# Kernel tuning notes

Hardware: AMD Instinct MI355X
Metric: run time of the kernel (lower is better)

The kernel has to match this reference:

```python
import jax, jax.numpy as jnp
import numpy as np

# Directable[TL_table[i]] for i = 0..7: (dx, dy) with dx=horizontal shift, dy=vertical shift
# dx=+1 -> shift right (zero-fill col 0), dx=-1 -> shift left; dy=+1 -> shift down, dy=-1 -> shift up.
DIRS = [(1, 1), (0, 1), (-1, 1), (1, 0), (-1, 0), (1, -1), (0, -1), (-1, -1)]


def _shift(img, dx, dy):
    # img: [B, H, W]; zero-padded shift equivalent to bmm with the sparse translation matrices
    if dx == 1:
        img = jnp.pad(img[..., :-1], ((0, 0), (0, 0), (1, 0)))
    elif dx == -1:
        img = jnp.pad(img[..., 1:], ((0, 0), (0, 0), (0, 1)))
    if dy == 1:
        img = jnp.pad(img[:, :-1, :], ((0, 0), (1, 0), (0, 0)))
    elif dy == -1:
        img = jnp.pad(img[:, 1:, :], ((0, 0), (0, 1), (0, 0)))
    return img


def _bce(p, t):
    # torch F.binary_cross_entropy clamps log terms at -100
    logp = jnp.maximum(jnp.log(p), -100.0)
    log1mp = jnp.maximum(jnp.log(1.0 - p), -100.0)
    return -jnp.mean(t * logp + (1.0 - t) * log1mp)


def setup_inputs() -> dict:
    key = jax.random.key(0)
    k1, k2, k3 = jax.random.split(key, 3)
    B, C, H, W = 16, 8, 512, 512
    c_map = jax.random.normal(k1, (B, C, H, W), dtype=jnp.float32)
    target = jax.random.randint(k2, (B, 1, H, W), 0, 2, dtype=jnp.int32)
    con_target = jax.random.randint(k3, (B, C, H, W), 0, 2, dtype=jnp.int32)
    return {"c_map": c_map, "target": target, "con_target": con_target}


def reference(c_map, target, con_target):
    target = target.astype(jnp.float32)        # [B,1,H,W]
    con_target = con_target.astype(jnp.float32)  # [B,8,H,W]

    p = jax.nn.sigmoid(c_map)  # [B,8,H,W]

    # Bilateral voting: shifted[i] = shift(p[:, 7-i]) in direction DIRS[i]
    shifted = jnp.stack(
        [_shift(p[:, 7 - i], dx, dy) for i, (dx, dy) in enumerate(DIRS)], axis=1
    )  # [B,8,H,W]
    vote_out = p * shifted                       # [B,8,H,W] (== bimap.squeeze(1))
    final_pred = jnp.max(vote_out, axis=1, keepdims=True)  # [B,1,H,W]

    # dice loss (sums over dims (1,2) of the 4D tensors, as in the original)
    smooth = 0.001
    i_sum = jnp.sum(target, axis=(1, 2))
    j_sum = jnp.sum(final_pred, axis=(1, 2))
    inter = jnp.sum(target * final_pred, axis=(1, 2))
    loss_dice = jnp.mean(1.0 - (2.0 * inter + smooth) / (i_sum + j_sum + smooth))

    # edge (decouple) loss
    sum_conn = jnp.sum(con_target, axis=1)  # [B,H,W]
    edge = ((sum_conn < 8) & (sum_conn > 0)).astype(p.dtype)
    pred_min = jnp.min(vote_out, axis=1) * edge
    decouple_loss = _bce(pred_min, jnp.zeros_like(pred_min))

    bce_loss = _bce(final_pred, target)
    conmap_l = _bce(p, con_target)
    bimap_l = _bce(vote_out, con_target)

    return 0.8 * conmap_l + decouple_loss + 0.2 * bimap_l + bce_loss + loss_dice
```

## Files before the change

### kernel.cpp

```cpp
#include <hip/hip_runtime.h>

namespace {
constexpr int Bn = 16, Hn = 512, Wn = 512;
constexpr int HW  = Hn * Wn;
constexpr int CHW = 8 * HW;
constexpr int NCOL = Bn * Wn;
constexpr int ROWS = 8;
constexpr int GX   = Hn / ROWS;
constexpr int NBLK = GX * Bn;
constexpr int FBLK = 32;

__device__ __forceinline__ float frcp(float x) { return __builtin_amdgcn_rcpf(x); }

typedef float f4u __attribute__((ext_vector_type(4), aligned(4)));
}


__global__ __launch_bounds__(256, 4) void bicon_main(
    const float* __restrict__ c_map,
    const int*   __restrict__ target,
    const int*   __restrict__ con_target,
    float* __restrict__ col_i, float* __restrict__ col_j, float* __restrict__ col_x,
    double* __restrict__ bscal)
{
    const int tid  = threadIdx.x;
    const int lane = tid & 63;
    const int wv   = tid >> 6;
    const int half = wv & 1;
    const int rofs = wv >> 1;
    const int b    = blockIdx.y;
    const int h0   = blockIdx.x * ROWS;
    const int wq   = half * 256 + lane * 4;

    const float* cm = c_map      + (size_t)b * CHW;
    const int*   ct = con_target + (size_t)b * CHW;
    const int*   tg = target     + (size_t)b * HW;

    float s_con = 0.f, s_bi = 0.f, s_bce = 0.f, s_dec = 0.f;
    float ci[4] = {0, 0, 0, 0}, cj[4] = {0, 0, 0, 0}, cx[4] = {0, 0, 0, 0};

#pragma unroll 1
    for (int r = 0; r < ROWS / 2; ++r) {
        const int h    = h0 + 2 * r + rofs;
        const int base = h * Wn + wq;

        unsigned lo = 0u;
#pragma unroll
        for (int c = 0; c < 8; ++c) {
            const int4 u = *(const int4*)(ct + c * HW + base);
            lo |= ((unsigned)u.x << c)        | ((unsigned)u.y << (8 + c)) |
                  ((unsigned)u.z << (16 + c)) | ((unsigned)u.w << (24 + c));
        }

        float vmax[4], vmin[4];
#pragma unroll
        for (int k = 0; k < 4; ++k) { vmax[k] = 0.f; vmin[k] = 2.f; }

        auto center = [&](int c, float s[4]) {
            const float4 v = *(const float4*)(cm + c * HW + base);
            const float xs[4] = {v.x, v.y, v.z, v.w};
#pragma unroll
            for (int k = 0; k < 4; ++k) {
                const float e = __expf(-xs[k]);
                const float d = 1.f + e;
                s[k] = frcp(d);
                const float logd = __logf(d);
                s_con += fmaxf(((lo >> (8 * k + c)) & 1u) ? -logd : (-xs[k] - logd),
                               -100.f);
            }
        };
        auto nbr = [&](int c, int dy, int dx, float n[4]) {
            const int hn = h + dy;
            if ((unsigned)hn < (unsigned)Hn) {
                const f4u v = *(const f4u*)(cm + c * HW + hn * Wn + (wq + dx));
                const float xs[4] = {v.x, v.y, v.z, v.w};
#pragma unroll
                for (int k = 0; k < 4; ++k) n[k] = frcp(1.f + __expf(-xs[k]));
                if (dx == 1 && wq == Wn - 4) n[3] = 0.f;
                if (dx == -1 && wq == 0)     n[0] = 0.f;
            } else {
#pragma unroll
                for (int k = 0; k < 4; ++k) n[k] = 0.f;
            }
        };
        auto vote = [&](int i, const float si[4], const float nn[4]) {
#pragma unroll
            for (int k = 0; k < 4; ++k) {
                const float v = si[k] * nn[k];
                vmax[k] = fmaxf(vmax[k], v);
                vmin[k] = fminf(vmin[k], v);
                s_bi += fmaxf(__logf(((lo >> (8 * k + i)) & 1u) ? v : 1.f - v),
                              -100.f);
            }
        };

        {
            float pa[4], pb[4], na[4], nb_[4];
            center(0, pa); center(7, pb);
            nbr(0, +1, +1, na);  vote(7, pb, na);
            nbr(7, -1, -1, nb_); vote(0, pa, nb_);
        }
        {
            float pa[4], pb[4], na[4], nb_[4];
            center(1, pa); center(6, pb);
            nbr(1, +1, 0, na);   vote(6, pb, na);
            nbr(6, -1, 0, nb_);  vote(1, pa, nb_);
        }
        {
            float pa[4], pb[4], na[4], nb_[4];
            center(2, pa); center(5, pb);
            nbr(2, +1, -1, na);  vote(5, pb, na);
            nbr(5, -1, +1, nb_); vote(2, pa, nb_);
        }
        {
            float pa[4], pb[4], na[4], nb_[4];
            center(3, pa); center(4, pb);
            nbr(3, 0, +1, na);   vote(4, pb, na);
            nbr(4, 0, -1, nb_);  vote(3, pa, nb_);
        }

        const int4 t = *(const int4*)(tg + base);
        const int tk[4] = {t.x, t.y, t.z, t.w};
#pragma unroll
        for (int k = 0; k < 4; ++k) {
            const float fm = vmax[k];
            s_bce += fmaxf(__logf(tk[k] ? fm : 1.f - fm), -100.f);
            const int sc = __popc((int)((lo >> (8 * k)) & 0xffu));
            s_dec += (sc > 0 && sc < 8) ? fmaxf(__logf(1.f - vmin[k]), -100.f) : 0.f;
            ci[k] += (float)tk[k];
            cj[k] += fm;
            cx[k] += tk[k] ? fm : 0.f;
        }
    }

    __shared__ float cred[3][4][256];
#pragma unroll
    for (int k = 0; k < 4; ++k) {
        cred[0][wv][(lane << 2) + k] = ci[k];
        cred[1][wv][(lane << 2) + k] = cj[k];
        cred[2][wv][(lane << 2) + k] = cx[k];
    }

#pragma unroll
    for (int off = 32; off > 0; off >>= 1) {
        s_con += __shfl_down(s_con, off);
        s_bi  += __shfl_down(s_bi,  off);
        s_bce += __shfl_down(s_bce, off);
        s_dec += __shfl_down(s_dec, off);
    }
    __shared__ float wred[4][4];
    if (lane == 0) {
        wred[wv][0] = s_con; wred[wv][1] = s_bi;
        wred[wv][2] = s_bce; wred[wv][3] = s_dec;
    }
    __syncthreads();

#pragma unroll
    for (int j = tid; j < 512; j += 256) {
        const int hj = j >> 8, cidx = j & 255;
        const float a0 = cred[0][hj][cidx] + cred[0][hj + 2][cidx];
        const float a1 = cred[1][hj][cidx] + cred[1][hj + 2][cidx];
        const float a2 = cred[2][hj][cidx] + cred[2][hj + 2][cidx];
        atomicAdd(&col_i[b * Wn + j], a0);
        atomicAdd(&col_j[b * Wn + j], a1);
        atomicAdd(&col_x[b * Wn + j], a2);
    }
    if (tid < 4) {
        bscal[((size_t)blockIdx.y * GX + blockIdx.x) * 4 + tid] =
            (double)(wred[0][tid] + wred[1][tid] + wred[2][tid] + wred[3][tid]);
    }
}

__global__ __launch_bounds__(256) void bicon_finish(
    const float* __restrict__ col_i,
    const float* __restrict__ col_j,
    const float* __restrict__ col_x,
    const double* __restrict__ bscal,
    float* __restrict__ out)
{
    const int tid = threadIdx.x;
    const int col = blockIdx.x * 256 + tid;

    double part;
    {
        const float fi = col_i[col], fj = col_j[col], fx = col_x[col];
        part = (1.0 - (2.0 * (double)fx + 0.001) /
                      ((double)fi + (double)fj + 0.001)) / 8192.0;
    }
    if (tid < 32) {
        const int s = blockIdx.x * 32 + tid;
        const double c0 = bscal[s * 4 + 0], c1 = bscal[s * 4 + 1];
        const double c2 = bscal[s * 4 + 2], c3 = bscal[s * 4 + 3];
        part += -0.8 * c0 / 33554432.0 - 0.2 * c1 / 33554432.0
                - c2 / 4194304.0 - c3 / 4194304.0;
    }
#pragma unroll
    for (int off = 32; off > 0; off >>= 1) part += __shfl_down(part, off);
    __shared__ double red[4];
    if ((tid & 63) == 0) red[tid >> 6] = part;
    __syncthreads();
    if (tid == 0) atomicAdd(out, (float)(red[0] + red[1] + red[2] + red[3]));
}

extern "C" void kernel_launch(void* const* d_in, const int* in_sizes, int n_in,
                              void* d_out, int out_size, void* d_ws, size_t ws_size,
                              hipStream_t stream) {
    const float* c_map      = (const float*)d_in[0];
    const int*   target     = (const int*)d_in[1];
    const int*   con_target = (const int*)d_in[2];
    float* out = (float*)d_out;

    char* ws = (char*)d_ws;
    float*  col_i = (float*)ws;
    float*  col_j = col_i + NCOL;
    float*  col_x = col_j + NCOL;
    double* bscal = (double*)(ws + 3 * NCOL * sizeof(float));

    hipMemsetAsync(d_ws, 0, 3 * NCOL * sizeof(float), stream);
    hipMemsetAsync(d_out, 0, sizeof(float), stream);

    dim3 grid(GX, Bn);
    dim3 block(256);
    bicon_main<<<grid, block, 0, stream>>>(c_map, target, con_target,
                                           col_i, col_j, col_x, bscal);
    bicon_finish<<<FBLK, 256, 0, stream>>>(col_i, col_j, col_x, bscal, out);
}
```

Baseline: 352.0 us.

## Walk consecutive rows per wave, reusing neighbor sigmoids in registers

Each wave now processes four consecutive rows instead of interleaved rows. It carries sigmoids of channels 0-2 from the next row and channels 5-7 from the previous row in registers, so the vertically shifted neighbors are not reloaded and recomputed. Horizontal shifts are built from the center vectors plus one scalar boundary load each, which replaces the unaligned float4 loads. This cuts roughly half the exp/rcp work and neighbor memory traffic, at the cost of higher register pressure. The launch-bounds occupancy hint is also dropped.

```diff
diff --git a/kernel.cpp b/kernel.cpp
--- a/kernel.cpp
+++ b/kernel.cpp
@@ -5,18 +5,18 @@
 constexpr int HW  = Hn * Wn;
 constexpr int CHW = 8 * HW;
 constexpr int NCOL = Bn * Wn;
-constexpr int ROWS = 8;
-constexpr int GX   = Hn / ROWS;
+constexpr int WALK = 4;
+constexpr int ROWSB = 2 * WALK;
+constexpr int GX   = Hn / ROWSB;
 constexpr int NBLK = GX * Bn;
 constexpr int FBLK = 32;
 
 __device__ __forceinline__ float frcp(float x) { return __builtin_amdgcn_rcpf(x); }
-
-typedef float f4u __attribute__((ext_vector_type(4), aligned(4)));
-}
-
-
-__global__ __launch_bounds__(256, 4) void bicon_main(
+__device__ __forceinline__ float fsig(float x) { return frcp(1.f + __expf(-x)); }
+}
+
+
+__global__ __launch_bounds__(256) void bicon_main(
     const float* __restrict__ c_map,
     const int*   __restrict__ target,
     const int*   __restrict__ con_target,
@@ -27,9 +27,9 @@
     const int lane = tid & 63;
     const int wv   = tid >> 6;
     const int half = wv & 1;
-    const int rofs = wv >> 1;
+    const int rg   = wv >> 1;
     const int b    = blockIdx.y;
-    const int h0   = blockIdx.x * ROWS;
+    const int hstart = blockIdx.x * ROWSB + rg * WALK;
     const int wq   = half * 256 + lane * 4;
 
     const float* cm = c_map      + (size_t)b * CHW;
@@ -39,10 +39,48 @@
     float s_con = 0.f, s_bi = 0.f, s_bce = 0.f, s_dec = 0.f;
     float ci[4] = {0, 0, 0, 0}, cj[4] = {0, 0, 0, 0}, cx[4] = {0, 0, 0, 0};
 
+    auto sig4 = [&](const float4& v, float s[4]) {
+        s[0] = fsig(v.x); s[1] = fsig(v.y); s[2] = fsig(v.z); s[3] = fsig(v.w);
+    };
+
+    float C0[4], C1[4], C2[4];
+    float P5[4], P6[4], P7[4];
+    {
+        const int pb = hstart * Wn + wq;
+        sig4(*(const float4*)(cm + 0 * HW + pb), C0);
+        sig4(*(const float4*)(cm + 1 * HW + pb), C1);
+        sig4(*(const float4*)(cm + 2 * HW + pb), C2);
+    }
+    if (hstart > 0) {
+        const int pb = (hstart - 1) * Wn + wq;
+        sig4(*(const float4*)(cm + 5 * HW + pb), P5);
+        sig4(*(const float4*)(cm + 6 * HW + pb), P6);
+        sig4(*(const float4*)(cm + 7 * HW + pb), P7);
+    } else {
+#pragma unroll
+        for (int k = 0; k < 4; ++k) { P5[k] = 0.f; P6[k] = 0.f; P7[k] = 0.f; }
+    }
+
+    const bool edR = (wq + 4 == Wn);
+    const bool edL = (wq == 0);
+
+    int h = hstart;
 #pragma unroll 1
-    for (int r = 0; r < ROWS / 2; ++r) {
-        const int h    = h0 + 2 * r + rofs;
-        const int base = h * Wn + wq;
+    for (int r = 0; r < WALK; ++r, ++h) {
+        const int  base  = h * Wn + wq;
+        const bool hasDn = (h + 1 < Hn);
+        const bool hasUp = (h > 0);
+
+        const float4 xf0 = *(const float4*)(cm + 0 * HW + base + Wn);
+        const float4 xf1 = *(const float4*)(cm + 1 * HW + base + Wn);
+        const float4 xf2 = *(const float4*)(cm + 2 * HW + base + Wn);
+        const float bx0 = cm[0 * HW + base + Wn + 4];
+        const float bx2 = cm[2 * HW + base + Wn - 1];
+        const float bx3 = cm[3 * HW + base + 4];
+        const float bx4 = cm[4 * HW + base - 1];
+        const float bx5 = cm[5 * HW + base - Wn + 4];
+        const float bx7 = cm[7 * HW + base - Wn - 1];
+        const int4 t4  = *(const int4*)(tg + base);
 
         unsigned lo = 0u;
 #pragma unroll
@@ -52,11 +90,15 @@
                   ((unsigned)u.z << (16 + c)) | ((unsigned)u.w << (24 + c));
         }
 
-        float vmax[4], vmin[4];
-#pragma unroll
-        for (int k = 0; k < 4; ++k) { vmax[k] = 0.f; vmin[k] = 2.f; }
-
-        auto center = [&](int c, float s[4]) {
+#pragma unroll
+        for (int k = 0; k < 4; ++k) {
+            s_con += fmaxf(__logf(((lo >> (8 * k + 0)) & 1u) ? C0[k] : 1.f - C0[k]), -100.f);
+            s_con += fmaxf(__logf(((lo >> (8 * k + 1)) & 1u) ? C1[k] : 1.f - C1[k]), -100.f);
+            s_con += fmaxf(__logf(((lo >> (8 * k + 2)) & 1u) ? C2[k] : 1.f - C2[k]), -100.f);
+        }
+
+        float c3[4], c4[4], c5[4], c6[4], c7[4];
+        auto sigcon = [&](int c, float s[4]) {
             const float4 v = *(const float4*)(cm + c * HW + base);
             const float xs[4] = {v.x, v.y, v.z, v.w};
 #pragma unroll
@@ -69,67 +111,61 @@
                                -100.f);
             }
         };
-        auto nbr = [&](int c, int dy, int dx, float n[4]) {
-            const int hn = h + dy;
-            if ((unsigned)hn < (unsigned)Hn) {
-                const f4u v = *(const f4u*)(cm + c * HW + hn * Wn + (wq + dx));
-                const float xs[4] = {v.x, v.y, v.z, v.w};
-#pragma unroll
-                for (int k = 0; k < 4; ++k) n[k] = frcp(1.f + __expf(-xs[k]));
-                if (dx == 1 && wq == Wn - 4) n[3] = 0.f;
-                if (dx == -1 && wq == 0)     n[0] = 0.f;
-            } else {
-#pragma unroll
-                for (int k = 0; k < 4; ++k) n[k] = 0.f;
-            }
-        };
-        auto vote = [&](int i, const float si[4], const float nn[4]) {
+        sigcon(3, c3); sigcon(4, c4); sigcon(5, c5); sigcon(6, c6); sigcon(7, c7);
+
+        float F0[4], F1[4], F2[4];
+        sig4(xf0, F0); sig4(xf1, F1); sig4(xf2, F2);
+
+        const float s0b = fsig(bx0), s2b = fsig(bx2), s3b = fsig(bx3);
+        const float s4b = fsig(bx4), s5b = fsig(bx5), s7b = fsig(bx7);
+
+        float n0[4], n1[4], n2[4], n3[4], n4[4], n5[4], n6[4], n7[4];
+#pragma unroll
+        for (int k = 0; k < 3; ++k) {
+            n0[k] = F0[k + 1]; n3[k] = c3[k + 1]; n5[k] = P5[k + 1];
+            n2[k + 1] = F2[k]; n4[k + 1] = c4[k]; n7[k + 1] = P7[k];
+        }
+        n0[3] = edR ? 0.f : s0b;  n3[3] = edR ? 0.f : s3b;  n5[3] = edR ? 0.f : s5b;
+        n2[0] = edL ? 0.f : s2b;  n4[0] = edL ? 0.f : s4b;  n7[0] = edL ? 0.f : s7b;
+#pragma unroll
+        for (int k = 0; k < 4; ++k) {
+            n1[k] = hasDn ? F1[k] : 0.f;
+            n6[k] = hasUp ? P6[k] : 0.f;
+            if (!hasDn) { n0[k] = 0.f; n2[k] = 0.f; }
+            if (!hasUp) { n5[k] = 0.f; n7[k] = 0.f; }
+        }
+
+        float vmax[4] = {0.f, 0.f, 0.f, 0.f}, vmin[4] = {2.f, 2.f, 2.f, 2.f};
+        auto vote = [&](int i, const float p[4], const float n[4]) {
 #pragma unroll
             for (int k = 0; k < 4; ++k) {
-                const float v = si[k] * nn[k];
+                const float v = p[k] * n[k];
                 vmax[k] = fmaxf(vmax[k], v);
                 vmin[k] = fminf(vmin[k], v);
                 s_bi += fmaxf(__logf(((lo >> (8 * k + i)) & 1u) ? v : 1.f - v),
                               -100.f);
             }
         };
-
-        {
-            float pa[4], pb[4], na[4], nb_[4];
-            center(0, pa); center(7, pb);
-            nbr(0, +1, +1, na);  vote(7, pb, na);
-            nbr(7, -1, -1, nb_); vote(0, pa, nb_);
-        }
-        {
-            float pa[4], pb[4], na[4], nb_[4];
-            center(1, pa); center(6, pb);
-            nbr(1, +1, 0, na);   vote(6, pb, na);
-            nbr(6, -1, 0, nb_);  vote(1, pa, nb_);
-        }
-        {
-            float pa[4], pb[4], na[4], nb_[4];
-            center(2, pa); center(5, pb);
-            nbr(2, +1, -1, na);  vote(5, pb, na);
-            nbr(5, -1, +1, nb_); vote(2, pa, nb_);
-        }
-        {
-            float pa[4], pb[4], na[4], nb_[4];
-            center(3, pa); center(4, pb);
-            nbr(3, 0, +1, na);   vote(4, pb, na);
-            nbr(4, 0, -1, nb_);  vote(3, pa, nb_);
-        }
-
-        const int4 t = *(const int4*)(tg + base);
-        const int tk[4] = {t.x, t.y, t.z, t.w};
+        vote(0, C0, n7); vote(1, C1, n6); vote(2, C2, n5); vote(3, c3, n4);
+        vote(4, c4, n3); vote(5, c5, n2); vote(6, c6, n1); vote(7, c7, n0);
+
+        const int tk[4] = {t4.x, t4.y, t4.z, t4.w};
 #pragma unroll
         for (int k = 0; k < 4; ++k) {
             const float fm = vmax[k];
             s_bce += fmaxf(__logf(tk[k] ? fm : 1.f - fm), -100.f);
             const int sc = __popc((int)((lo >> (8 * k)) & 0xffu));
-            s_dec += (sc > 0 && sc < 8) ? fmaxf(__logf(1.f - vmin[k]), -100.f) : 0.f;
+            s_dec += (sc > 0 && sc < 8)
+                         ? fmaxf(__logf(1.f - vmin[k]), -100.f) : 0.f;
             ci[k] += (float)tk[k];
             cj[k] += fm;
             cx[k] += tk[k] ? fm : 0.f;
+        }
+
+#pragma unroll
+        for (int k = 0; k < 4; ++k) {
+            C0[k] = F0[k]; C1[k] = F1[k]; C2[k] = F2[k];
+            P5[k] = c5[k]; P6[k] = c6[k]; P7[k] = c7[k];
         }
     }
 
```

Result: faster. 308.1 us (-12.5%).
